# Kernel optimization log

Hardware: AMD Instinct MI355X
Metric: run time of the kernel (lower is better)

Reference implementation:

```python
import jax, jax.numpy as jnp
import numpy as np

B, L = 64, 2048
N_RESTYPE, N_GROUP, N_ATOM = 21, 8, 14


def _compose(R1, t1, R2, t2):
    # rigid compose: (R1,t1) o (R2,t2) = (R1@R2, R1@t2 + t1)
    R = jnp.einsum('...ij,...jk->...ik', R1, R2)
    t = jnp.einsum('...ij,...j->...i', R1, t2) + t1
    return R, t


def setup_inputs() -> dict:
    key = jax.random.key(0)
    ks = jax.random.split(key, 8)
    return {
        'bb_rots': jax.random.normal(ks[0], (B, L, 3, 3), jnp.float32),
        'bb_trans': jax.random.normal(ks[1], (B, L, 3), jnp.float32),
        'angles': jax.random.normal(ks[2], (B, L, 7, 2), jnp.float32),
        'aatype': jax.random.randint(ks[3], (B, L), 0, N_RESTYPE),
        'default_frames': jax.random.normal(ks[4], (N_RESTYPE, N_GROUP, 4, 4), jnp.float32),
        'group_idx': jax.random.randint(ks[5], (N_RESTYPE, N_ATOM), 0, N_GROUP),
        'atom_mask': jax.random.uniform(ks[6], (N_RESTYPE, N_ATOM), jnp.float32),
        'lit_positions': jax.random.normal(ks[7], (N_RESTYPE, N_ATOM, 3), jnp.float32),
    }


def reference(bb_rots, bb_trans, angles, aatype, default_frames, group_idx, atom_mask, lit_positions):
    # ---- torsion_angles_to_frames ----
    d4 = default_frames[aatype]                      # [B,L,8,4,4]
    dR, dt = d4[..., :3, :3], d4[..., :3, 3]
    # prepend identity backbone torsion (sin=0, cos=1)
    bb = jnp.broadcast_to(jnp.array([0.0, 1.0], angles.dtype), (*angles.shape[:-2], 1, 2))
    ang = jnp.concatenate([bb, angles], axis=-2)     # [B,L,8,2]
    s, c = ang[..., 0], ang[..., 1]
    z, o = jnp.zeros_like(s), jnp.ones_like(s)
    # rotation about x-axis built from (sin, cos)
    rotx = jnp.stack([
        jnp.stack([o, z, z], axis=-1),
        jnp.stack([z, c, -s], axis=-1),
        jnp.stack([z, s, c], axis=-1),
    ], axis=-2)                                      # [B,L,8,3,3]
    fR = jnp.einsum('blgij,blgjk->blgik', dR, rotx)  # default_r.compose(all_rots)
    ft = dt                                          # all_rots has zero translation
    # chain chi2..chi4 onto chi1
    R5, t5 = _compose(fR[:, :, 4], ft[:, :, 4], fR[:, :, 5], ft[:, :, 5])
    R6, t6 = _compose(R5, t5, fR[:, :, 6], ft[:, :, 6])
    R7, t7 = _compose(R6, t6, fR[:, :, 7], ft[:, :, 7])
    Rbb = jnp.concatenate([fR[:, :, :5], R5[:, :, None], R6[:, :, None], R7[:, :, None]], axis=2)
    tbb = jnp.concatenate([ft[:, :, :5], t5[:, :, None], t6[:, :, None], t7[:, :, None]], axis=2)
    # compose with global backbone frame
    Rg = jnp.einsum('blij,blgjk->blgik', bb_rots, Rbb)          # [B,L,8,3,3]
    tg = jnp.einsum('blij,blgj->blgi', bb_rots, tbb) + bb_trans[:, :, None]

    # ---- frames_and_literature_positions_to_atom14_pos ----
    gidx = group_idx[aatype]                                    # [B,L,14]
    Ra = jnp.take_along_axis(Rg, gidx[:, :, :, None, None], axis=2)  # [B,L,14,3,3]
    ta = jnp.take_along_axis(tg, gidx[:, :, :, None], axis=2)        # [B,L,14,3]
    lit = lit_positions[aatype]                                 # [B,L,14,3]
    mask = atom_mask[aatype][..., None]                         # [B,L,14,1]
    pred = jnp.einsum('blaij,blaj->blai', Ra, lit) + ta
    return pred * mask
```

## Files before the change

kernel.cpp:

```cpp
#include <hip/hip_runtime.h>


constexpr int NRES_TOTAL = 64 * 2048;
constexpr int NRT = 21;
constexpr int NG  = 8;
constexpr int NA  = 14;

__global__ __launch_bounds__(256, 2) void protein_mapper_kernel(
    const float* __restrict__ bb_rots,
    const float* __restrict__ bb_trans,
    const float* __restrict__ angles,
    const int*   __restrict__ aatype,
    const float* __restrict__ default_frames,
    const int*   __restrict__ group_idx,
    const float* __restrict__ atom_mask,
    const float* __restrict__ lit_positions,
    float* __restrict__ out)
{
    __shared__ float s_frames[128 * NRT];
    __shared__ int   s_gidx[NA * NRT];
    __shared__ float s_mask[NA * NRT];
    __shared__ float s_lit[NA * 3 * NRT];

    for (int n = threadIdx.x; n < NRT * 128; n += 256) {
        const int aa = n / 128, j = n % 128;
        s_frames[j * NRT + aa] = default_frames[n];
    }
    for (int n = threadIdx.x; n < NRT * NA; n += 256) {
        const int aa = n / NA, a = n % NA;
        s_gidx[a * NRT + aa] = group_idx[n];
        s_mask[a * NRT + aa] = atom_mask[n];
    }
    for (int n = threadIdx.x; n < NRT * NA * 3; n += 256) {
        const int aa = n / (NA * 3), k = n % (NA * 3);
        s_lit[k * NRT + aa] = lit_positions[n];
    }
    __syncthreads();

    const int i = blockIdx.x * 256 + threadIdx.x;
    const int aa = aatype[i];

    float sv[NG], cv[NG];
    sv[0] = 0.0f; cv[0] = 1.0f;
    const float2* angp = reinterpret_cast<const float2*>(angles + (size_t)i * 14);
    #pragma unroll
    for (int g = 1; g < NG; ++g) {
        float2 sc = angp[g - 1];
        sv[g] = sc.x;
        cv[g] = sc.y;
    }

    float G[NG][12];
    #pragma unroll
    for (int g = 0; g < NG; ++g) {
        const float cg = cv[g], sg = sv[g];
        #pragma unroll
        for (int r = 0; r < 3; ++r) {
            const float a0 = s_frames[(g * 16 + r * 4 + 0) * NRT + aa];
            const float a1 = s_frames[(g * 16 + r * 4 + 1) * NRT + aa];
            const float a2 = s_frames[(g * 16 + r * 4 + 2) * NRT + aa];
            const float a3 = s_frames[(g * 16 + r * 4 + 3) * NRT + aa];
            G[g][r * 3 + 0] = a0;
            G[g][r * 3 + 1] = cg * a1 + sg * a2;
            G[g][r * 3 + 2] = cg * a2 - sg * a1;
            G[g][9 + r]     = a3;
        }
    }

    #pragma unroll
    for (int g = 5; g < NG; ++g) {
        float Q[12];
        #pragma unroll
        for (int r = 0; r < 3; ++r) {
            const float p0 = G[g - 1][r * 3 + 0];
            const float p1 = G[g - 1][r * 3 + 1];
            const float p2 = G[g - 1][r * 3 + 2];
            #pragma unroll
            for (int cdx = 0; cdx < 3; ++cdx)
                Q[r * 3 + cdx] = p0 * G[g][cdx] + p1 * G[g][3 + cdx] + p2 * G[g][6 + cdx];
            Q[9 + r] = p0 * G[g][9] + p1 * G[g][10] + p2 * G[g][11] + G[g - 1][9 + r];
        }
        #pragma unroll
        for (int k = 0; k < 12; ++k) G[g][k] = Q[k];
    }

    const float* br = bb_rots + (size_t)i * 9;
    const float b00 = br[0], b01 = br[1], b02 = br[2];
    const float b10 = br[3], b11 = br[4], b12 = br[5];
    const float b20 = br[6], b21 = br[7], b22 = br[8];
    const float* btp = bb_trans + (size_t)i * 3;
    const float bt0 = btp[0], bt1 = btp[1], bt2 = btp[2];

    auto atom_pos = [&](int a, float& qx, float& qy, float& qz) {
        const int   ga = s_gidx[a * NRT + aa];
        const float m_ = s_mask[a * NRT + aa];
        const float lx = s_lit[(a * 3 + 0) * NRT + aa];
        const float ly = s_lit[(a * 3 + 1) * NRT + aa];
        const float lz = s_lit[(a * 3 + 2) * NRT + aa];
        const bool b0_ = ga & 1, b1_ = ga & 2, b2_ = ga & 4;
        float S[12];
        #pragma unroll
        for (int e = 0; e < 12; ++e) {
            const float t0 = b0_ ? G[1][e] : G[0][e];
            const float t1 = b0_ ? G[3][e] : G[2][e];
            const float t2 = b0_ ? G[5][e] : G[4][e];
            const float t3 = b0_ ? G[7][e] : G[6][e];
            const float u0 = b1_ ? t1 : t0;
            const float u1 = b1_ ? t3 : t2;
            S[e] = b2_ ? u1 : u0;
        }
        const float px = S[0] * lx + S[1] * ly + S[2] * lz + S[9];
        const float py = S[3] * lx + S[4] * ly + S[5] * lz + S[10];
        const float pz = S[6] * lx + S[7] * ly + S[8] * lz + S[11];
        qx = (b00 * px + b01 * py + b02 * pz + bt0) * m_;
        qy = (b10 * px + b11 * py + b12 * pz + bt1) * m_;
        qz = (b20 * px + b21 * py + b22 * pz + bt2) * m_;
    };

    float2* op2 = reinterpret_cast<float2*>(out + (size_t)i * (NA * 3));
    #pragma unroll
    for (int ap = 0; ap < NA / 2; ++ap) {
        float qx0, qy0, qz0, qx1, qy1, qz1;
        atom_pos(2 * ap + 0, qx0, qy0, qz0);
        atom_pos(2 * ap + 1, qx1, qy1, qz1);
        float2 v0; v0.x = qx0; v0.y = qy0;
        float2 v1; v1.x = qz0; v1.y = qx1;
        float2 v2; v2.x = qy1; v2.y = qz1;
        op2[3 * ap + 0] = v0;
        op2[3 * ap + 1] = v1;
        op2[3 * ap + 2] = v2;
    }
}

extern "C" void kernel_launch(void* const* d_in, const int* in_sizes, int n_in,
                              void* d_out, int out_size, void* d_ws, size_t ws_size,
                              hipStream_t stream) {
    const float* bb_rots        = (const float*)d_in[0];
    const float* bb_trans       = (const float*)d_in[1];
    const float* angles         = (const float*)d_in[2];
    const int*   aatype         = (const int*)d_in[3];
    const float* default_frames = (const float*)d_in[4];
    const int*   group_idx      = (const int*)d_in[5];
    const float* atom_mask      = (const float*)d_in[6];
    const float* lit_positions  = (const float*)d_in[7];
    float* out = (float*)d_out;

    const int blocks = NRES_TOTAL / 256;
    protein_mapper_kernel<<<blocks, 256, 0, stream>>>(
        bb_rots, bb_trans, angles, aatype,
        default_frames, group_idx, atom_mask, lit_positions, out);
}
```

Before: 96.67 us.

## Stream group frames through a rolled loop and select atom positions per group

The kernel no longer keeps all eight group frames live in registers. A rolled loop over groups computes each frame, chaining groups 5-7 through a running composite, and conditionally assigns every atom whose group index matches. This lowers register pressure at the cost of recomputing 14 atom transforms per group, and the global loads of aatype and angles are moved ahead of the shared-memory table fill so they overlap with it. The kernel is memory-bound, so the extra arithmetic (about 8x more atom transforms) may or may not be hidden.

```diff
diff --git a/kernel.cpp b/kernel.cpp
--- a/kernel.cpp
+++ b/kernel.cpp
@@ -22,66 +22,98 @@
     __shared__ float s_mask[NA * NRT];
     __shared__ float s_lit[NA * 3 * NRT];
 
+    const int i  = blockIdx.x * 256 + threadIdx.x;
+    const int aa = aatype[i];
+    float sv[NG], cv[NG];
+    sv[0] = 0.0f; cv[0] = 1.0f;
+    {
+        const float2* angp = reinterpret_cast<const float2*>(angles + (size_t)i * 14);
+        #pragma unroll
+        for (int g = 1; g < NG; ++g) {
+            float2 sc = angp[g - 1];
+            sv[g] = sc.x;
+            cv[g] = sc.y;
+        }
+    }
+
     for (int n = threadIdx.x; n < NRT * 128; n += 256) {
-        const int aa = n / 128, j = n % 128;
-        s_frames[j * NRT + aa] = default_frames[n];
+        const int a_ = n / 128, j = n % 128;
+        s_frames[j * NRT + a_] = default_frames[n];
     }
     for (int n = threadIdx.x; n < NRT * NA; n += 256) {
-        const int aa = n / NA, a = n % NA;
-        s_gidx[a * NRT + aa] = group_idx[n];
-        s_mask[a * NRT + aa] = atom_mask[n];
+        const int a_ = n / NA, a = n % NA;
+        s_gidx[a * NRT + a_] = group_idx[n];
+        s_mask[a * NRT + a_] = atom_mask[n];
     }
     for (int n = threadIdx.x; n < NRT * NA * 3; n += 256) {
-        const int aa = n / (NA * 3), k = n % (NA * 3);
-        s_lit[k * NRT + aa] = lit_positions[n];
+        const int a_ = n / (NA * 3), k = n % (NA * 3);
+        s_lit[k * NRT + a_] = lit_positions[n];
     }
     __syncthreads();
 
-    const int i = blockIdx.x * 256 + threadIdx.x;
-    const int aa = aatype[i];
+    int ga[NA];
+    #pragma unroll
+    for (int a = 0; a < NA; ++a) ga[a] = s_gidx[a * NRT + aa];
 
-    float sv[NG], cv[NG];
-    sv[0] = 0.0f; cv[0] = 1.0f;
-    const float2* angp = reinterpret_cast<const float2*>(angles + (size_t)i * 14);
+    float p[NA * 3];
     #pragma unroll
-    for (int g = 1; g < NG; ++g) {
-        float2 sc = angp[g - 1];
-        sv[g] = sc.x;
-        cv[g] = sc.y;
-    }
+    for (int k = 0; k < NA * 3; ++k) p[k] = 0.0f;
 
-    float G[NG][12];
-    #pragma unroll
+    float C[12];
+    #pragma clang loop unroll(disable)
     for (int g = 0; g < NG; ++g) {
-        const float cg = cv[g], sg = sv[g];
+        float sg_ = sv[0], cg_ = cv[0];
+        sg_ = (g == 1) ? sv[1] : sg_;  cg_ = (g == 1) ? cv[1] : cg_;
+        sg_ = (g == 2) ? sv[2] : sg_;  cg_ = (g == 2) ? cv[2] : cg_;
+        sg_ = (g == 3) ? sv[3] : sg_;  cg_ = (g == 3) ? cv[3] : cg_;
+        sg_ = (g == 4) ? sv[4] : sg_;  cg_ = (g == 4) ? cv[4] : cg_;
+        sg_ = (g == 5) ? sv[5] : sg_;  cg_ = (g == 5) ? cv[5] : cg_;
+        sg_ = (g == 6) ? sv[6] : sg_;  cg_ = (g == 6) ? cv[6] : cg_;
+        sg_ = (g == 7) ? sv[7] : sg_;  cg_ = (g == 7) ? cv[7] : cg_;
+
+        float L[12];
         #pragma unroll
         for (int r = 0; r < 3; ++r) {
             const float a0 = s_frames[(g * 16 + r * 4 + 0) * NRT + aa];
             const float a1 = s_frames[(g * 16 + r * 4 + 1) * NRT + aa];
             const float a2 = s_frames[(g * 16 + r * 4 + 2) * NRT + aa];
             const float a3 = s_frames[(g * 16 + r * 4 + 3) * NRT + aa];
-            G[g][r * 3 + 0] = a0;
-            G[g][r * 3 + 1] = cg * a1 + sg * a2;
-            G[g][r * 3 + 2] = cg * a2 - sg * a1;
-            G[g][9 + r]     = a3;
+            L[r * 3 + 0] = a0;
+            L[r * 3 + 1] = cg_ * a1 + sg_ * a2;
+            L[r * 3 + 2] = cg_ * a2 - sg_ * a1;
+            L[9 + r]     = a3;
         }
-    }
 
-    #pragma unroll
-    for (int g = 5; g < NG; ++g) {
-        float Q[12];
+        if (g < 5) {
+            #pragma unroll
+            for (int k = 0; k < 12; ++k) C[k] = L[k];
+        } else {
+            float Q[12];
+            #pragma unroll
+            for (int r = 0; r < 3; ++r) {
+                const float c0 = C[r * 3 + 0], c1 = C[r * 3 + 1], c2 = C[r * 3 + 2];
+                #pragma unroll
+                for (int c = 0; c < 3; ++c)
+                    Q[r * 3 + c] = c0 * L[c] + c1 * L[3 + c] + c2 * L[6 + c];
+                Q[9 + r] = c0 * L[9] + c1 * L[10] + c2 * L[11] + C[9 + r];
+            }
+            #pragma unroll
+            for (int k = 0; k < 12; ++k) C[k] = Q[k];
+        }
+
         #pragma unroll
-        for (int r = 0; r < 3; ++r) {
-            const float p0 = G[g - 1][r * 3 + 0];
-            const float p1 = G[g - 1][r * 3 + 1];
-            const float p2 = G[g - 1][r * 3 + 2];
-            #pragma unroll
-            for (int cdx = 0; cdx < 3; ++cdx)
-                Q[r * 3 + cdx] = p0 * G[g][cdx] + p1 * G[g][3 + cdx] + p2 * G[g][6 + cdx];
-            Q[9 + r] = p0 * G[g][9] + p1 * G[g][10] + p2 * G[g][11] + G[g - 1][9 + r];
+        for (int a = 0; a < NA; ++a) {
+            const bool sel = (ga[a] == g);
+            const float lx = s_lit[(a * 3 + 0) * NRT + aa];
+            const float ly = s_lit[(a * 3 + 1) * NRT + aa];
+            const float lz = s_lit[(a * 3 + 2) * NRT + aa];
+            const float rx = C[0] * lx + C[1] * ly + C[2] * lz + C[9];
+            const float ry = C[3] * lx + C[4] * ly + C[5] * lz + C[10];
+            const float rz = C[6] * lx + C[7] * ly + C[8] * lz + C[11];
+            p[a * 3 + 0] = sel ? rx : p[a * 3 + 0];
+            p[a * 3 + 1] = sel ? ry : p[a * 3 + 1];
+            p[a * 3 + 2] = sel ? rz : p[a * 3 + 2];
         }
-        #pragma unroll
-        for (int k = 0; k < 12; ++k) G[g][k] = Q[k];
     }
 
     const float* br = bb_rots + (size_t)i * 9;
@@ -91,44 +123,21 @@
     const float* btp = bb_trans + (size_t)i * 3;
     const float bt0 = btp[0], bt1 = btp[1], bt2 = btp[2];
 
-    auto atom_pos = [&](int a, float& qx, float& qy, float& qz) {
-        const int   ga = s_gidx[a * NRT + aa];
+    float res[NA * 3];
+    #pragma unroll
+    for (int a = 0; a < NA; ++a) {
         const float m_ = s_mask[a * NRT + aa];
-        const float lx = s_lit[(a * 3 + 0) * NRT + aa];
-        const float ly = s_lit[(a * 3 + 1) * NRT + aa];
-        const float lz = s_lit[(a * 3 + 2) * NRT + aa];
-        const bool b0_ = ga & 1, b1_ = ga & 2, b2_ = ga & 4;
-        float S[12];
-        #pragma unroll
-        for (int e = 0; e < 12; ++e) {
-            const float t0 = b0_ ? G[1][e] : G[0][e];
-            const float t1 = b0_ ? G[3][e] : G[2][e];
-            const float t2 = b0_ ? G[5][e] : G[4][e];
-            const float t3 = b0_ ? G[7][e] : G[6][e];
-            const float u0 = b1_ ? t1 : t0;
-            const float u1 = b1_ ? t3 : t2;
-            S[e] = b2_ ? u1 : u0;
-        }
-        const float px = S[0] * lx + S[1] * ly + S[2] * lz + S[9];
-        const float py = S[3] * lx + S[4] * ly + S[5] * lz + S[10];
-        const float pz = S[6] * lx + S[7] * ly + S[8] * lz + S[11];
-        qx = (b00 * px + b01 * py + b02 * pz + bt0) * m_;
-        qy = (b10 * px + b11 * py + b12 * pz + bt1) * m_;
-        qz = (b20 * px + b21 * py + b22 * pz + bt2) * m_;
-    };
+        const float px = p[a * 3 + 0], py = p[a * 3 + 1], pz = p[a * 3 + 2];
+        res[a * 3 + 0] = (b00 * px + b01 * py + b02 * pz + bt0) * m_;
+        res[a * 3 + 1] = (b10 * px + b11 * py + b12 * pz + bt1) * m_;
+        res[a * 3 + 2] = (b20 * px + b21 * py + b22 * pz + bt2) * m_;
+    }
 
     float2* op2 = reinterpret_cast<float2*>(out + (size_t)i * (NA * 3));
     #pragma unroll
-    for (int ap = 0; ap < NA / 2; ++ap) {
-        float qx0, qy0, qz0, qx1, qy1, qz1;
-        atom_pos(2 * ap + 0, qx0, qy0, qz0);
-        atom_pos(2 * ap + 1, qx1, qy1, qz1);
-        float2 v0; v0.x = qx0; v0.y = qy0;
-        float2 v1; v1.x = qz0; v1.y = qx1;
-        float2 v2; v2.x = qy1; v2.y = qz1;
-        op2[3 * ap + 0] = v0;
-        op2[3 * ap + 1] = v1;
-        op2[3 * ap + 2] = v2;
+    for (int k = 0; k < (NA * 3) / 2; ++k) {
+        float2 v; v.x = res[2 * k + 0]; v.y = res[2 * k + 1];
+        op2[k] = v;
     }
 }
 
```

Result: no change. 96.78 us (+0.1%).
